# Kernel tuning notes

Measured on AMD Instinct MI355X. Metric: run time of the kernel, lower is better.

## Reference

```python
import jax, jax.numpy as jnp
import numpy as np

B, S, E, H = 2, 2048, 1024, 16
D = E // H


def setup_inputs() -> dict:
    key = jax.random.key(0)
    ks = jax.random.split(key, 8)
    q = jax.random.normal(ks[0], (B, S, E), dtype=jnp.float32)
    k = jax.random.normal(ks[1], (B, S, E), dtype=jnp.float32)
    v = jax.random.normal(ks[2], (B, S, E), dtype=jnp.float32)
    mask = jax.random.randint(ks[3], (B, 1, 1, S), 0, 2, dtype=jnp.int32)
    sc = 1.0 / np.sqrt(E)
    W_qkv = jax.random.normal(ks[4], (3 * E, E), dtype=jnp.float32) * sc
    b_qkv = jnp.zeros((3 * E,), dtype=jnp.float32)
    W_out = jax.random.normal(ks[5], (E, E), dtype=jnp.float32) * sc
    b_out = jnp.zeros((E,), dtype=jnp.float32)
    return {"q": q, "k": k, "v": v, "mask": mask,
            "W_qkv": W_qkv, "b_qkv": b_qkv, "W_out": W_out, "b_out": b_out}


def reference(q, k, v, mask, W_qkv, b_qkv, W_out, b_out):
    # Fused qkv linear: q takes the Q-slice, k the K-slice, v the V-slice.
    qp = (q @ W_qkv[:E].T + b_qkv[:E]).reshape(B, S, H, D)
    kp = (k @ W_qkv[E:2 * E].T + b_qkv[E:2 * E]).reshape(B, S, H, D)
    vp = (v @ W_qkv[2 * E:].T + b_qkv[2 * E:]).reshape(B, S, H, D)
    # (B,H,S,S) scores -- NOTE: original module does NOT scale by sqrt(d)
    energy = jnp.einsum('nqhd,nkhd->nhqk', qp, kp)
    energy = jnp.where(mask == 0, jnp.float32(-1e20), energy)
    attention = jax.nn.softmax(energy, axis=-1)
    out = jnp.einsum('nhql,nlhd->nqhd', attention, vp).reshape(B, S, E)
    return out @ W_out.T + b_out
```

## Files before the change

### kernel.cpp

```cpp
#include <hip/hip_runtime.h>
#include <stdint.h>

constexpr int B_ = 2, S_ = 2048, E_ = 1024, H_ = 16, D_ = 64;
constexpr int M_ = B_ * S_;

typedef unsigned short u16;
typedef __attribute__((ext_vector_type(8))) short short8;
typedef __attribute__((ext_vector_type(4))) float f32x4;

__device__ __forceinline__ u16 f2bf(float f) {
  uint32_t u = __float_as_uint(f);
  return (u16)((u + 0x7FFFu + ((u >> 16) & 1u)) >> 16);
}
__device__ __forceinline__ void tsplit(float x, u16& hi, u16& lo) {
  const uint32_t u = __float_as_uint(x);
  hi = (u16)(u >> 16);
  const float hif = __uint_as_float(u & 0xFFFF0000u);
  lo = (u16)(__float_as_uint(x - hif) >> 16);
}

__global__ __launch_bounds__(256) void split_f32_kernel(
    const float* __restrict__ src, u16* __restrict__ hi, u16* __restrict__ lo, int n4)
{
  const int i = blockIdx.x * 256 + threadIdx.x;
  if (i >= n4) return;
  const float4 x = ((const float4*)src)[i];
  ushort4 h, l;
  tsplit(x.x, h.x, l.x); tsplit(x.y, h.y, l.y);
  tsplit(x.z, h.z, l.z); tsplit(x.w, h.w, l.w);
  ((ushort4*)hi)[i] = h;
  ((ushort4*)lo)[i] = l;
}

__global__ __launch_bounds__(256) void mask_scan_kernel(
    const int* __restrict__ mask, int* __restrict__ opos, int* __restrict__ nk)
{
  __shared__ int tmp[256];
  __shared__ int coff;
  const int b = blockIdx.x, t = threadIdx.x;
  for (int c = t; c < S_; c += 256) opos[b * S_ + c] = 0;
  if (t == 0) coff = 0;
  __syncthreads();
  for (int c = 0; c < S_; c += 256) {
    const int m = (mask[b * S_ + c + t] != 0) ? 1 : 0;
    int x = m;
    tmp[t] = x;
    __syncthreads();
#pragma unroll
    for (int off = 1; off < 256; off <<= 1) {
      const int v = (t >= off) ? tmp[t - off] : 0;
      __syncthreads();
      x += v;
      tmp[t] = x;
      __syncthreads();
    }
    const int base = coff;
    if (m) opos[b * S_ + base + x - 1] = c + t;
    __syncthreads();
    if (t == 255) coff = base + x;
    __syncthreads();
  }
  if (t == 0) nk[b] = coff;
}

__global__ __launch_bounds__(256) void gemm_qkv_kernel(
    const float* __restrict__ q, const float* __restrict__ k, const float* __restrict__ v,
    const u16* __restrict__ WHi, const u16* __restrict__ WLo,
    const float* __restrict__ bias,
    const int* __restrict__ Opos, const int* __restrict__ NkArr,
    u16* __restrict__ QpHi, u16* __restrict__ QpLo,
    u16* __restrict__ KpHi, u16* __restrict__ KpLo,
    u16* __restrict__ Vp)
{
  __shared__ __align__(16) short smem[15360];
  short* Ah = smem;
  short* Al = smem + 5120;
  short* Bh = smem + 10240;
  short* Bl = smem + 12800;

  const int t = threadIdx.x;
  const int m0 = blockIdx.x * 128;
  const int n0g = blockIdx.y * 64;
  const int proj = n0g >> 10;
  const int nloc = n0g & (E_ - 1);
  const bool split = (proj < 2);
  const int bb = m0 >> 11, mloc = m0 & (S_ - 1);
  const int nkb = NkArr[bb];
  if (proj != 0 && mloc >= nkb) return;

  const float* A = (proj == 0) ? q : (proj == 1) ? k : v;

  const int w = t >> 6, lane = t & 63;
  const int g = lane >> 4, lc = lane & 15;
  const int wm = w & 1, wn = w >> 1;
  const int sra = t >> 1, sca = (t & 1) * 16;
  const int srb = t >> 2, scb = (t & 3) * 8;

  int arow;
  if (proj == 0) arow = m0 + sra;
  else arow = bb * S_ + (Opos[bb * S_ + mloc + sra] & (S_ - 1));
  const float* Abp = A + (size_t)arow * E_ + sca;
  const u16* Bhb = WHi + (size_t)(n0g + srb) * E_ + scb;
  const u16* Blb = WLo + (size_t)(n0g + srb) * E_ + scb;

  f32x4 acc[4][2];
#pragma unroll
  for (int i = 0; i < 4; ++i)
#pragma unroll
    for (int j = 0; j < 2; ++j) acc[i][j] = (f32x4){0.f, 0.f, 0.f, 0.f};

  float4 ar[4]; short8 br, cr;
#pragma unroll
  for (int i = 0; i < 4; ++i) ar[i] = *(const float4*)(Abp + 4 * i);
  br = *(const short8*)(Bhb);
  if (split) cr = *(const short8*)(Blb);

  for (int k0 = 0; k0 < E_; k0 += 32) {
    __syncthreads();
#pragma unroll
    for (int i = 0; i < 4; ++i) {
      ushort4 h, l;
      tsplit(ar[i].x, h.x, l.x); tsplit(ar[i].y, h.y, l.y);
      tsplit(ar[i].z, h.z, l.z); tsplit(ar[i].w, h.w, l.w);
      *(ushort4*)&Ah[sra * 40 + sca + 4 * i] = h;
      if (split) *(ushort4*)&Al[sra * 40 + sca + 4 * i] = l;
    }
    *(short8*)&Bh[srb * 40 + scb] = br;
    if (split) *(short8*)&Bl[srb * 40 + scb] = cr;
    __syncthreads();
    if (k0 + 32 < E_) {
#pragma unroll
      for (int i = 0; i < 4; ++i) ar[i] = *(const float4*)(Abp + k0 + 32 + 4 * i);
      br = *(const short8*)(Bhb + k0 + 32);
      if (split) cr = *(const short8*)(Blb + k0 + 32);
    }

    short8 ah[4], al[4], bh[2], bl[2];
#pragma unroll
    for (int mt = 0; mt < 4; ++mt) {
      const int ro = (wm * 64 + mt * 16 + lc) * 40 + g * 8;
      ah[mt] = *(const short8*)&Ah[ro];
      if (split) al[mt] = *(const short8*)&Al[ro];
    }
#pragma unroll
    for (int nt = 0; nt < 2; ++nt) {
      const int ro = (wn * 32 + nt * 16 + lc) * 40 + g * 8;
      bh[nt] = *(const short8*)&Bh[ro];
      if (split) bl[nt] = *(const short8*)&Bl[ro];
    }
#pragma unroll
    for (int mt = 0; mt < 4; ++mt)
#pragma unroll
      for (int nt = 0; nt < 2; ++nt) {
        f32x4 a = acc[mt][nt];
        a = __builtin_amdgcn_mfma_f32_16x16x32_bf16(ah[mt], bh[nt], a, 0, 0, 0);
        if (split) {
          a = __builtin_amdgcn_mfma_f32_16x16x32_bf16(ah[mt], bl[nt], a, 0, 0, 0);
          a = __builtin_amdgcn_mfma_f32_16x16x32_bf16(al[mt], bh[nt], a, 0, 0, 0);
        }
        acc[mt][nt] = a;
      }
  }

  float bs[2];
#pragma unroll
  for (int nt = 0; nt < 2; ++nt) bs[nt] = bias[n0g + wn * 32 + nt * 16 + lc];

  if (proj < 2) {
    u16* Hi = (proj == 0) ? QpHi : KpHi;
    u16* Lo = (proj == 0) ? QpLo : KpLo;
    const int head = nloc >> 6;
    short* T = smem + w * 2560;
    const int s = (m0 + wm * 64 + lane) & (S_ - 1);
    const size_t rowb = (((size_t)(bb * H_ + head)) * S_ + s) * D_ + wn * 32;
#pragma unroll
    for (int pass = 0; pass < 2; ++pass) {
      __syncthreads();
#pragma unroll
      for (int nt = 0; nt < 2; ++nt)
#pragma unroll
        for (int mt = 0; mt < 4; ++mt)
#pragma unroll
          for (int r = 0; r < 4; ++r) {
            const float val = acc[mt][nt][r] + bs[nt];
            const uint32_t u = __float_as_uint(val);
            u16 x;
            if (pass == 0) x = (u16)(u >> 16);
            else {
              const float hif = __uint_as_float(u & 0xFFFF0000u);
              x = (u16)(__float_as_uint(val - hif) >> 16);
            }
            T[(mt * 16 + g * 4 + r) * 40 + nt * 16 + lc] = (short)x;
          }
      __syncthreads();
      u16* dst = (pass == 0) ? Hi : Lo;
#pragma unroll
      for (int j = 0; j < 4; ++j)
        *(short8*)&dst[rowb + 8 * j] = *(const short8*)&T[lane * 40 + 8 * j];
    }
  } else {
#pragma unroll
    for (int mt = 0; mt < 4; ++mt) {
      const int jb = mloc + wm * 64 + mt * 16 + g * 4;
#pragma unroll
      for (int nt = 0; nt < 2; ++nt) {
        const int nE = nloc + wn * 32 + nt * 16 + lc;
        const int h = nE >> 6, d = nE & 63;
        const size_t rb = (((size_t)(bb * H_ + h)) * D_ + d) * S_;
#pragma unroll
        for (int r = 0; r < 4; ++r) {
          if (jb + r < nkb) Vp[rb + jb + r] = f2bf(acc[mt][nt][r] + bs[nt]);
        }
      }
    }
  }
}

__global__ __launch_bounds__(256, 4) void attn_mfma_kernel(
    const u16* __restrict__ QpHi, const u16* __restrict__ QpLo,
    const u16* __restrict__ KpHi, const u16* __restrict__ KpLo,
    const u16* __restrict__ Vp,
    const int* __restrict__ nkArr,
    u16* __restrict__ AOHi)
{
  __shared__ __align__(16) short sm[18432];
  short* Khi = sm;
  short* Klo = sm + 4608;
  short* Vt  = sm + 9216;
  short* Pb  = sm + 13824;

  const int t = threadIdx.x;
  const int w = t >> 6, lane = t & 63;
  const int g = lane >> 4, lc = lane & 15;
  const int bh = blockIdx.y;
  const int b = bh >> 4, hh = bh & 15;
  const int q0 = blockIdx.x * 64;
  const size_t hb = (size_t)bh * S_ * D_;
  const u16* QgH = QpHi + hb;
  const u16* QgL = QpLo + hb;
  const u16* KgH = KpHi + hb;
  const u16* KgL = KpLo + hb;
  const u16* Vg  = Vp + hb;
  short* Pw = Pb + w * 1152;

  const int nk = nkArr[b];
  const int kend = ((nk + 63) >> 6) << 6;

  short8 qh[2], ql[2];
  {
    const size_t base = (size_t)(q0 + 16 * w + lc) * D_ + 8 * g;
    qh[0] = *(const short8*)&QgH[base];
    qh[1] = *(const short8*)&QgH[base + 32];
    ql[0] = *(const short8*)&QgL[base];
    ql[1] = *(const short8*)&QgL[base + 32];
  }

  short8 ones8 = {0, 0, 0, 0, 0, 0, 0, 0};
  if (lc == 0) {
    const short o = (short)0x3F80;
    ones8 = (short8){o, o, o, o, o, o, o, o};
  }

  f32x4 O[4];
  f32x4 Ol = (f32x4){0.f, 0.f, 0.f, 0.f};
#pragma unroll
  for (int dt = 0; dt < 4; ++dt) O[dt] = (f32x4){0.f, 0.f, 0.f, 0.f};
  float mst[4] = {-INFINITY, -INFINITY, -INFINITY, -INFINITY};

  const int srow = t >> 2, sc16 = (t & 3) * 16;

  short8 kr[2], lr[2], vr[2];
  kr[0] = *(const short8*)&KgH[srow * D_ + sc16];
  kr[1] = *(const short8*)&KgH[srow * D_ + sc16 + 8];
  lr[0] = *(const short8*)&KgL[srow * D_ + sc16];
  lr[1] = *(const short8*)&KgL[srow * D_ + sc16 + 8];
  vr[0] = *(const short8*)&Vg[srow * S_ + sc16];
  vr[1] = *(const short8*)&Vg[srow * S_ + sc16 + 8];

  for (int kt = 0; kt < kend; kt += 64) {
    __syncthreads();
    *(short8*)&Khi[srow * 72 + sc16]     = kr[0];
    *(short8*)&Khi[srow * 72 + sc16 + 8] = kr[1];
    *(short8*)&Klo[srow * 72 + sc16]     = lr[0];
    *(short8*)&Klo[srow * 72 + sc16 + 8] = lr[1];
    *(short8*)&Vt[srow * 72 + sc16]      = vr[0];
    *(short8*)&Vt[srow * 72 + sc16 + 8]  = vr[1];
    __syncthreads();
    if (kt + 64 < kend) {
      const int kn = kt + 64;
      kr[0] = *(const short8*)&KgH[(kn + srow) * D_ + sc16];
      kr[1] = *(const short8*)&KgH[(kn + srow) * D_ + sc16 + 8];
      lr[0] = *(const short8*)&KgL[(kn + srow) * D_ + sc16];
      lr[1] = *(const short8*)&KgL[(kn + srow) * D_ + sc16 + 8];
      vr[0] = *(const short8*)&Vg[srow * S_ + kn + sc16];
      vr[1] = *(const short8*)&Vg[srow * S_ + kn + sc16 + 8];
    }

    f32x4 sc[4];
#pragma unroll
    for (int kt16 = 0; kt16 < 4; ++kt16) {
      const int ko = (16 * kt16 + lc) * 72 + 8 * g;
      const short8 kh0 = *(const short8*)&Khi[ko];
      const short8 kh1 = *(const short8*)&Khi[ko + 32];
      const short8 kl0 = *(const short8*)&Klo[ko];
      const short8 kl1 = *(const short8*)&Klo[ko + 32];
      f32x4 a = {0.f, 0.f, 0.f, 0.f};
      a = __builtin_amdgcn_mfma_f32_16x16x32_bf16(qh[0], kh0, a, 0, 0, 0);
      a = __builtin_amdgcn_mfma_f32_16x16x32_bf16(qh[1], kh1, a, 0, 0, 0);
      a = __builtin_amdgcn_mfma_f32_16x16x32_bf16(qh[0], kl0, a, 0, 0, 0);
      a = __builtin_amdgcn_mfma_f32_16x16x32_bf16(qh[1], kl1, a, 0, 0, 0);
      a = __builtin_amdgcn_mfma_f32_16x16x32_bf16(ql[0], kh0, a, 0, 0, 0);
      a = __builtin_amdgcn_mfma_f32_16x16x32_bf16(ql[1], kh1, a, 0, 0, 0);
      sc[kt16] = a;
    }

    if (kt + 64 > nk) {
#pragma unroll
      for (int kt16 = 0; kt16 < 4; ++kt16) {
        if (kt + 16 * kt16 + lc >= nk) {
          sc[kt16][0] = -1e20f; sc[kt16][1] = -1e20f;
          sc[kt16][2] = -1e20f; sc[kt16][3] = -1e20f;
        }
      }
    }

    float al[4];
#pragma unroll
    for (int r = 0; r < 4; ++r) {
      float vv = fmaxf(fmaxf(sc[0][r], sc[1][r]), fmaxf(sc[2][r], sc[3][r]));
      vv = fmaxf(vv, __shfl_xor(vv, 1));
      vv = fmaxf(vv, __shfl_xor(vv, 2));
      vv = fmaxf(vv, __shfl_xor(vv, 4));
      vv = fmaxf(vv, __shfl_xor(vv, 8));
      const float mn = fmaxf(mst[r], vv);
      al[r] = __expf(mst[r] - mn);
      mst[r] = mn;
    }
#pragma unroll
    for (int kt16 = 0; kt16 < 4; ++kt16) {
#pragma unroll
      for (int r = 0; r < 4; ++r)
        sc[kt16][r] = __expf(sc[kt16][r] - mst[r]);
    }
    const f32x4 alv = {al[0], al[1], al[2], al[3]};
    O[0] *= alv; O[1] *= alv; O[2] *= alv; O[3] *= alv;
    Ol *= alv;
#pragma unroll
    for (int kt16 = 0; kt16 < 4; ++kt16) {
#pragma unroll
      for (int r = 0; r < 4; ++r)
        Pw[(4 * g + r) * 72 + 16 * kt16 + lc] = (short)f2bf(sc[kt16][r]);
    }

    short8 pa[2];
    pa[0] = *(const short8*)&Pw[lc * 72 + 8 * g];
    pa[1] = *(const short8*)&Pw[lc * 72 + 32 + 8 * g];
    Ol = __builtin_amdgcn_mfma_f32_16x16x32_bf16(pa[0], ones8, Ol, 0, 0, 0);
    Ol = __builtin_amdgcn_mfma_f32_16x16x32_bf16(pa[1], ones8, Ol, 0, 0, 0);
#pragma unroll
    for (int dt = 0; dt < 4; ++dt) {
      const int vo = (16 * dt + lc) * 72 + 8 * g;
      const short8 vb0 = *(const short8*)&Vt[vo];
      const short8 vb1 = *(const short8*)&Vt[vo + 32];
      O[dt] = __builtin_amdgcn_mfma_f32_16x16x32_bf16(pa[0], vb0, O[dt], 0, 0, 0);
      O[dt] = __builtin_amdgcn_mfma_f32_16x16x32_bf16(pa[1], vb1, O[dt], 0, 0, 0);
    }
  }

#pragma unroll
  for (int r = 0; r < 4; ++r) {
    const float lv = __shfl(Ol[r], lane & 48);
    const float lir = 1.0f / lv;
    const int qrow = q0 + 16 * w + 4 * g + r;
    const size_t rowb = (size_t)(b * S_ + qrow) * E_ + hh * 64;
#pragma unroll
    for (int dt = 0; dt < 4; ++dt)
      AOHi[rowb + dt * 16 + lc] = f2bf(O[dt][r] * lir);
  }
}

__global__ __launch_bounds__(256) void gemm_out_kernel(
    const u16* __restrict__ AHi,
    const u16* __restrict__ WHi,
    const float* __restrict__ bias, float* __restrict__ out)
{
  __shared__ __align__(16) short smem[5120];
  short* Ah = smem;
  short* Bh = smem + 2560;

  const int t = threadIdx.x;
  const int m0 = blockIdx.x * 64;
  const int n0 = blockIdx.y * 64;
  const int w = t >> 6, lane = t & 63;
  const int g = lane >> 4, lc = lane & 15;
  const int wm = w & 1, wn = w >> 1;
  const int sr = t >> 2, sc = (t & 3) * 8;

  const u16* Ahb = AHi + (size_t)(m0 + sr) * E_ + sc;
  const u16* Bhb = WHi + (size_t)(n0 + sr) * E_ + sc;

  f32x4 acc[2][2];
#pragma unroll
  for (int i = 0; i < 2; ++i)
#pragma unroll
    for (int j = 0; j < 2; ++j) acc[i][j] = (f32x4){0.f, 0.f, 0.f, 0.f};

  short8 arr, brr;
  arr = *(const short8*)(Ahb);
  brr = *(const short8*)(Bhb);

  for (int k0 = 0; k0 < E_; k0 += 32) {
    __syncthreads();
    *(short8*)&Ah[sr * 40 + sc] = arr;
    *(short8*)&Bh[sr * 40 + sc] = brr;
    __syncthreads();
    if (k0 + 32 < E_) {
      arr = *(const short8*)(Ahb + k0 + 32);
      brr = *(const short8*)(Bhb + k0 + 32);
    }

    short8 ah[2], bh[2];
#pragma unroll
    for (int mt = 0; mt < 2; ++mt)
      ah[mt] = *(const short8*)&Ah[(wm * 32 + mt * 16 + lc) * 40 + g * 8];
#pragma unroll
    for (int nt = 0; nt < 2; ++nt)
      bh[nt] = *(const short8*)&Bh[(wn * 32 + nt * 16 + lc) * 40 + g * 8];
#pragma unroll
    for (int mt = 0; mt < 2; ++mt)
#pragma unroll
      for (int nt = 0; nt < 2; ++nt)
        acc[mt][nt] = __builtin_amdgcn_mfma_f32_16x16x32_bf16(ah[mt], bh[nt], acc[mt][nt], 0, 0, 0);
  }

  float bs[2];
#pragma unroll
  for (int nt = 0; nt < 2; ++nt) bs[nt] = bias[n0 + wn * 32 + nt * 16 + lc];
#pragma unroll
  for (int nt = 0; nt < 2; ++nt) {
    const int nc = n0 + wn * 32 + nt * 16 + lc;
#pragma unroll
    for (int mt = 0; mt < 2; ++mt) {
#pragma unroll
      for (int r = 0; r < 4; ++r) {
        const int mrow = m0 + wm * 32 + mt * 16 + g * 4 + r;
        out[(size_t)mrow * E_ + nc] = acc[mt][nt][r] + bs[nt];
      }
    }
  }
}

extern "C" void kernel_launch(void* const* d_in, const int* in_sizes, int n_in,
                              void* d_out, int out_size, void* d_ws, size_t ws_size,
                              hipStream_t stream) {
  const float* q    = (const float*)d_in[0];
  const float* k    = (const float*)d_in[1];
  const float* v    = (const float*)d_in[2];
  const int*   mask = (const int*)d_in[3];
  const float* Wqkv = (const float*)d_in[4];
  const float* bqkv = (const float*)d_in[5];
  const float* Wout = (const float*)d_in[6];
  const float* bout = (const float*)d_in[7];
  float* out = (float*)d_out;

  char* wsb = (char*)d_ws;
  u16* WqkvHi = (u16*)(wsb + 0);
  u16* WqkvLo = (u16*)(wsb + 6291456);
  u16* WoutHi = (u16*)(wsb + 12582912);
  int* Opos   = (int*)(wsb + 14680064);
  int* Nk     = (int*)(wsb + 14680064 + 16384);
  u16* WoutLo = (u16*)(wsb + 14680064);
  u16* QpHi   = (u16*)(wsb + 16777216);
  u16* QpLo   = (u16*)(wsb + 25165824);
  u16* KpHi   = (u16*)(wsb + 33554432);
  u16* KpLo   = (u16*)(wsb + 41943040);
  u16* Vp     = (u16*)(wsb + 50331648);
  u16* AOHi   = (u16*)(wsb + 58720256);

  hipLaunchKernelGGL(split_f32_kernel, dim3(3072), dim3(256), 0, stream,
                     Wqkv, WqkvHi, WqkvLo, 786432);
  hipLaunchKernelGGL(split_f32_kernel, dim3(1024), dim3(256), 0, stream,
                     Wout, WoutHi, WoutLo, 262144);
  hipLaunchKernelGGL(mask_scan_kernel, dim3(B_), dim3(256), 0, stream,
                     mask, Opos, Nk);
  hipMemsetAsync(Vp, 0, 8388608, stream);
  hipLaunchKernelGGL(gemm_qkv_kernel, dim3(M_ / 128, 48), dim3(256), 0, stream,
                     q, k, v, WqkvHi, WqkvLo, bqkv, Opos, Nk,
                     QpHi, QpLo, KpHi, KpLo, Vp);
  hipLaunchKernelGGL(attn_mfma_kernel, dim3(S_ / 64, B_ * H_), dim3(256), 0, stream,
                     QpHi, QpLo, KpHi, KpLo, Vp, Nk, AOHi);
  hipLaunchKernelGGL(gemm_out_kernel, dim3(M_ / 64, E_ / 64), dim3(256), 0, stream,
                     AOHi, WoutHi, bout, out);
}
```

Before: 296.9 us.

## Load GEMM operands directly to registers, enlarge tiles, and relax attention barriers

Both projection GEMMs stop staging A/B tiles through shared memory. Each lane now loads its MFMA fragments straight from global memory, which removes the per-step __syncthreads pairs. The QKV GEMM tile grows to 128x128 with a 4x4 accumulator per wave, and the output GEMM tile grows to 128x64. The attention kernel swaps __syncthreads for an lgkmcnt wait plus s_barrier. The direct loads are strided 16-byte reads per lane that rely on cache for reuse instead of LDS, and the larger accumulators raise register pressure.

```diff
diff --git a/kernel.cpp b/kernel.cpp
--- a/kernel.cpp
+++ b/kernel.cpp
@@ -72,15 +72,11 @@
     u16* __restrict__ KpHi, u16* __restrict__ KpLo,
     u16* __restrict__ Vp)
 {
-  __shared__ __align__(16) short smem[15360];
-  short* Ah = smem;
-  short* Al = smem + 5120;
-  short* Bh = smem + 10240;
-  short* Bl = smem + 12800;
+  __shared__ __align__(16) short T[4 * 4608];
 
   const int t = threadIdx.x;
   const int m0 = blockIdx.x * 128;
-  const int n0g = blockIdx.y * 64;
+  const int n0g = blockIdx.y * 128;
   const int proj = n0g >> 10;
   const int nloc = n0g & (E_ - 1);
   const bool split = (proj < 2);
@@ -93,65 +89,65 @@
   const int w = t >> 6, lane = t & 63;
   const int g = lane >> 4, lc = lane & 15;
   const int wm = w & 1, wn = w >> 1;
-  const int sra = t >> 1, sca = (t & 1) * 16;
-  const int srb = t >> 2, scb = (t & 3) * 8;
-
-  int arow;
-  if (proj == 0) arow = m0 + sra;
-  else arow = bb * S_ + (Opos[bb * S_ + mloc + sra] & (S_ - 1));
-  const float* Abp = A + (size_t)arow * E_ + sca;
-  const u16* Bhb = WHi + (size_t)(n0g + srb) * E_ + scb;
-  const u16* Blb = WLo + (size_t)(n0g + srb) * E_ + scb;
-
-  f32x4 acc[4][2];
+
+  const float* Arow[4];
+#pragma unroll
+  for (int mt = 0; mt < 4; ++mt) {
+    int r;
+    if (proj == 0) r = m0 + wm * 64 + mt * 16 + lc;
+    else {
+      const int slot = mloc + wm * 64 + mt * 16 + lc;
+      r = bb * S_ + (Opos[bb * S_ + slot] & (S_ - 1));
+    }
+    Arow[mt] = A + (size_t)r * E_ + 8 * g;
+  }
+  const u16* BrowH[4];
+  const u16* BrowL[4];
+#pragma unroll
+  for (int nt = 0; nt < 4; ++nt) {
+    const int c = n0g + wn * 64 + nt * 16 + lc;
+    BrowH[nt] = WHi + (size_t)c * E_ + 8 * g;
+    BrowL[nt] = WLo + (size_t)c * E_ + 8 * g;
+  }
+
+  f32x4 acc[4][4];
 #pragma unroll
   for (int i = 0; i < 4; ++i)
 #pragma unroll
-    for (int j = 0; j < 2; ++j) acc[i][j] = (f32x4){0.f, 0.f, 0.f, 0.f};
-
-  float4 ar[4]; short8 br, cr;
-#pragma unroll
-  for (int i = 0; i < 4; ++i) ar[i] = *(const float4*)(Abp + 4 * i);
-  br = *(const short8*)(Bhb);
-  if (split) cr = *(const short8*)(Blb);
+    for (int j = 0; j < 4; ++j) acc[i][j] = (f32x4){0.f, 0.f, 0.f, 0.f};
 
   for (int k0 = 0; k0 < E_; k0 += 32) {
-    __syncthreads();
-#pragma unroll
-    for (int i = 0; i < 4; ++i) {
-      ushort4 h, l;
-      tsplit(ar[i].x, h.x, l.x); tsplit(ar[i].y, h.y, l.y);
-      tsplit(ar[i].z, h.z, l.z); tsplit(ar[i].w, h.w, l.w);
-      *(ushort4*)&Ah[sra * 40 + sca + 4 * i] = h;
-      if (split) *(ushort4*)&Al[sra * 40 + sca + 4 * i] = l;
-    }
-    *(short8*)&Bh[srb * 40 + scb] = br;
-    if (split) *(short8*)&Bl[srb * 40 + scb] = cr;
-    __syncthreads();
-    if (k0 + 32 < E_) {
-#pragma unroll
-      for (int i = 0; i < 4; ++i) ar[i] = *(const float4*)(Abp + k0 + 32 + 4 * i);
-      br = *(const short8*)(Bhb + k0 + 32);
-      if (split) cr = *(const short8*)(Blb + k0 + 32);
-    }
-
-    short8 ah[4], al[4], bh[2], bl[2];
+    short8 ah[4], al[4];
 #pragma unroll
     for (int mt = 0; mt < 4; ++mt) {
-      const int ro = (wm * 64 + mt * 16 + lc) * 40 + g * 8;
-      ah[mt] = *(const short8*)&Ah[ro];
-      if (split) al[mt] = *(const short8*)&Al[ro];
-    }
-#pragma unroll
-    for (int nt = 0; nt < 2; ++nt) {
-      const int ro = (wn * 32 + nt * 16 + lc) * 40 + g * 8;
-      bh[nt] = *(const short8*)&Bh[ro];
-      if (split) bl[nt] = *(const short8*)&Bl[ro];
+      const float4 xa = *(const float4*)(Arow[mt] + k0);
+      const float4 xb = *(const float4*)(Arow[mt] + k0 + 4);
+      const float xs[8] = {xa.x, xa.y, xa.z, xa.w, xb.x, xb.y, xb.z, xb.w};
+      short8 h8, l8;
+#pragma unroll
+      for (int j = 0; j < 8; ++j) {
+        const uint32_t u = __float_as_uint(xs[j]);
+        h8[j] = (short)(u >> 16);
+        if (split) {
+          const float hif = __uint_as_float(u & 0xFFFF0000u);
+          l8[j] = (short)(__float_as_uint(xs[j] - hif) >> 16);
+        } else {
+          l8[j] = 0;
+        }
+      }
+      ah[mt] = h8;
+      al[mt] = l8;
+    }
+    short8 bh[4], bl[4];
+#pragma unroll
+    for (int nt = 0; nt < 4; ++nt) {
+      bh[nt] = *(const short8*)(BrowH[nt] + k0);
+      if (split) bl[nt] = *(const short8*)(BrowL[nt] + k0);
     }
 #pragma unroll
     for (int mt = 0; mt < 4; ++mt)
 #pragma unroll
-      for (int nt = 0; nt < 2; ++nt) {
+      for (int nt = 0; nt < 4; ++nt) {
         f32x4 a = acc[mt][nt];
         a = __builtin_amdgcn_mfma_f32_16x16x32_bf16(ah[mt], bh[nt], a, 0, 0, 0);
         if (split) {
@@ -162,22 +158,21 @@
       }
   }
 
-  float bs[2];
-#pragma unroll
-  for (int nt = 0; nt < 2; ++nt) bs[nt] = bias[n0g + wn * 32 + nt * 16 + lc];
+  float bs[4];
+#pragma unroll
+  for (int nt = 0; nt < 4; ++nt) bs[nt] = bias[n0g + wn * 64 + nt * 16 + lc];
 
   if (proj < 2) {
     u16* Hi = (proj == 0) ? QpHi : KpHi;
     u16* Lo = (proj == 0) ? QpLo : KpLo;
-    const int head = nloc >> 6;
-    short* T = smem + w * 2560;
-    const int s = (m0 + wm * 64 + lane) & (S_ - 1);
-    const size_t rowb = (((size_t)(bb * H_ + head)) * S_ + s) * D_ + wn * 32;
+    const int head = (nloc >> 6) + wn;
+    short* Tw = T + w * 4608;
+    const int srow = mloc + wm * 64 + lane;
+    const size_t rowb = (((size_t)(bb * H_ + head)) * S_ + srow) * D_;
 #pragma unroll
     for (int pass = 0; pass < 2; ++pass) {
-      __syncthreads();
-#pragma unroll
-      for (int nt = 0; nt < 2; ++nt)
+#pragma unroll
+      for (int nt = 0; nt < 4; ++nt)
 #pragma unroll
         for (int mt = 0; mt < 4; ++mt)
 #pragma unroll
@@ -190,21 +185,20 @@
               const float hif = __uint_as_float(u & 0xFFFF0000u);
               x = (u16)(__float_as_uint(val - hif) >> 16);
             }
-            T[(mt * 16 + g * 4 + r) * 40 + nt * 16 + lc] = (short)x;
+            Tw[(mt * 16 + g * 4 + r) * 72 + nt * 16 + lc] = (short)x;
           }
-      __syncthreads();
       u16* dst = (pass == 0) ? Hi : Lo;
 #pragma unroll
-      for (int j = 0; j < 4; ++j)
-        *(short8*)&dst[rowb + 8 * j] = *(const short8*)&T[lane * 40 + 8 * j];
+      for (int j = 0; j < 8; ++j)
+        *(short8*)&dst[rowb + 8 * j] = *(const short8*)&Tw[lane * 72 + 8 * j];
     }
   } else {
 #pragma unroll
     for (int mt = 0; mt < 4; ++mt) {
       const int jb = mloc + wm * 64 + mt * 16 + g * 4;
 #pragma unroll
-      for (int nt = 0; nt < 2; ++nt) {
-        const int nE = nloc + wn * 32 + nt * 16 + lc;
+      for (int nt = 0; nt < 4; ++nt) {
+        const int nE = nloc + wn * 64 + nt * 16 + lc;
         const int h = nE >> 6, d = nE & 63;
         const size_t rb = (((size_t)(bb * H_ + h)) * D_ + d) * S_;
 #pragma unroll
@@ -214,6 +208,11 @@
       }
     }
   }
+}
+
+__device__ __forceinline__ void block_sync() {
+  asm volatile("s_waitcnt lgkmcnt(0)" ::: "memory");
+  __builtin_amdgcn_s_barrier();
 }
 
 __global__ __launch_bounds__(256, 4) void attn_mfma_kernel(
@@ -278,14 +277,14 @@
   vr[1] = *(const short8*)&Vg[srow * S_ + sc16 + 8];
 
   for (int kt = 0; kt < kend; kt += 64) {
-    __syncthreads();
+    block_sync();
     *(short8*)&Khi[srow * 72 + sc16]     = kr[0];
     *(short8*)&Khi[srow * 72 + sc16 + 8] = kr[1];
     *(short8*)&Klo[srow * 72 + sc16]     = lr[0];
     *(short8*)&Klo[srow * 72 + sc16 + 8] = lr[1];
     *(short8*)&Vt[srow * 72 + sc16]      = vr[0];
     *(short8*)&Vt[srow * 72 + sc16 + 8]  = vr[1];
-    __syncthreads();
+    block_sync();
     if (kt + 64 < kend) {
       const int kn = kt + 64;
       kr[0] = *(const short8*)&KgH[(kn + srow) * D_ + sc16];
@@ -384,50 +383,36 @@
     const u16* __restrict__ WHi,
     const float* __restrict__ bias, float* __restrict__ out)
 {
-  __shared__ __align__(16) short smem[5120];
-  short* Ah = smem;
-  short* Bh = smem + 2560;
-
   const int t = threadIdx.x;
-  const int m0 = blockIdx.x * 64;
+  const int m0 = blockIdx.x * 128;
   const int n0 = blockIdx.y * 64;
   const int w = t >> 6, lane = t & 63;
   const int g = lane >> 4, lc = lane & 15;
   const int wm = w & 1, wn = w >> 1;
-  const int sr = t >> 2, sc = (t & 3) * 8;
-
-  const u16* Ahb = AHi + (size_t)(m0 + sr) * E_ + sc;
-  const u16* Bhb = WHi + (size_t)(n0 + sr) * E_ + sc;
-
-  f32x4 acc[2][2];
-#pragma unroll
-  for (int i = 0; i < 2; ++i)
+
+  const u16* Arow[4];
+#pragma unroll
+  for (int mt = 0; mt < 4; ++mt)
+    Arow[mt] = AHi + (size_t)(m0 + wm * 64 + mt * 16 + lc) * E_ + 8 * g;
+  const u16* Brow[2];
+#pragma unroll
+  for (int nt = 0; nt < 2; ++nt)
+    Brow[nt] = WHi + (size_t)(n0 + wn * 32 + nt * 16 + lc) * E_ + 8 * g;
+
+  f32x4 acc[4][2];
+#pragma unroll
+  for (int i = 0; i < 4; ++i)
 #pragma unroll
     for (int j = 0; j < 2; ++j) acc[i][j] = (f32x4){0.f, 0.f, 0.f, 0.f};
 
-  short8 arr, brr;
-  arr = *(const short8*)(Ahb);
-  brr = *(const short8*)(Bhb);
-
   for (int k0 = 0; k0 < E_; k0 += 32) {
-    __syncthreads();
-    *(short8*)&Ah[sr * 40 + sc] = arr;
-    *(short8*)&Bh[sr * 40 + sc] = brr;
-    __syncthreads();
-    if (k0 + 32 < E_) {
-      arr = *(const short8*)(Ahb + k0 + 32);
-      brr = *(const short8*)(Bhb + k0 + 32);
-    }
-
-    short8 ah[2], bh[2];
-#pragma unroll
-    for (int mt = 0; mt < 2; ++mt)
-      ah[mt] = *(const short8*)&Ah[(wm * 32 + mt * 16 + lc) * 40 + g * 8];
-#pragma unroll
-    for (int nt = 0; nt < 2; ++nt)
-      bh[nt] = *(const short8*)&Bh[(wn * 32 + nt * 16 + lc) * 40 + g * 8];
-#pragma unroll
-    for (int mt = 0; mt < 2; ++mt)
+    short8 ah[4], bh[2];
+#pragma unroll
+    for (int mt = 0; mt < 4; ++mt) ah[mt] = *(const short8*)(Arow[mt] + k0);
+#pragma unroll
+    for (int nt = 0; nt < 2; ++nt) bh[nt] = *(const short8*)(Brow[nt] + k0);
+#pragma unroll
+    for (int mt = 0; mt < 4; ++mt)
 #pragma unroll
       for (int nt = 0; nt < 2; ++nt)
         acc[mt][nt] = __builtin_amdgcn_mfma_f32_16x16x32_bf16(ah[mt], bh[nt], acc[mt][nt], 0, 0, 0);
@@ -440,10 +425,10 @@
   for (int nt = 0; nt < 2; ++nt) {
     const int nc = n0 + wn * 32 + nt * 16 + lc;
 #pragma unroll
-    for (int mt = 0; mt < 2; ++mt) {
+    for (int mt = 0; mt < 4; ++mt) {
 #pragma unroll
       for (int r = 0; r < 4; ++r) {
-        const int mrow = m0 + wm * 32 + mt * 16 + g * 4 + r;
+        const int mrow = m0 + wm * 64 + mt * 16 + g * 4 + r;
         out[(size_t)mrow * E_ + nc] = acc[mt][nt][r] + bs[nt];
       }
     }
@@ -484,11 +469,11 @@
   hipLaunchKernelGGL(mask_scan_kernel, dim3(B_), dim3(256), 0, stream,
                      mask, Opos, Nk);
   hipMemsetAsync(Vp, 0, 8388608, stream);
-  hipLaunchKernelGGL(gemm_qkv_kernel, dim3(M_ / 128, 48), dim3(256), 0, stream,
+  hipLaunchKernelGGL(gemm_qkv_kernel, dim3(M_ / 128, 24), dim3(256), 0, stream,
                      q, k, v, WqkvHi, WqkvLo, bqkv, Opos, Nk,
                      QpHi, QpLo, KpHi, KpLo, Vp);
   hipLaunchKernelGGL(attn_mfma_kernel, dim3(S_ / 64, B_ * H_), dim3(256), 0, stream,
                      QpHi, QpLo, KpHi, KpLo, Vp, Nk, AOHi);
-  hipLaunchKernelGGL(gemm_out_kernel, dim3(M_ / 64, E_ / 64), dim3(256), 0, stream,
+  hipLaunchKernelGGL(gemm_out_kernel, dim3(M_ / 128, E_ / 64), dim3(256), 0, stream,
                      AOHi, WoutHi, bout, out);
 }
```

New measurement: 410.7 us. 1.38x slower.
